# Performance work log

Hardware: AMD Instinct MI355X
Metric: run time of the kernel (lower is better)

The kernel has to match this reference:

```python
import jax, jax.numpy as jnp
import numpy as np

N_NODES = 100000
N_EDGES = 3200000
IN_FEATS = 512
HIDDEN = 16
NUM_CLASSES = 40


def setup_inputs() -> dict:
    key = jax.random.key(0)
    k1, k2, k3, k4, k5, k6 = jax.random.split(key, 6)
    x = jax.random.normal(k1, (N_NODES, IN_FEATS), dtype=jnp.float32)
    edge_index = jax.random.randint(k2, (2, N_EDGES), 0, N_NODES, dtype=jnp.int64)
    # Glorot-ish init for GCN weights
    W1 = jax.random.normal(k3, (IN_FEATS, HIDDEN), dtype=jnp.float32) / np.sqrt(IN_FEATS)
    b1 = jnp.zeros((HIDDEN,), dtype=jnp.float32)
    W2 = jax.random.normal(k4, (HIDDEN, NUM_CLASSES), dtype=jnp.float32) / np.sqrt(HIDDEN)
    b2 = jnp.zeros((NUM_CLASSES,), dtype=jnp.float32)
    return {"x": x, "edge_index": edge_index, "W1": W1, "b1": b1, "W2": W2, "b2": b2}


def _gcn_norm(edge_index, num_nodes):
    # Add self-loops (PyG GCNConv default), then symmetric normalization
    loops = jnp.arange(num_nodes, dtype=edge_index.dtype)
    src = jnp.concatenate([edge_index[0], loops])
    dst = jnp.concatenate([edge_index[1], loops])
    deg = jax.ops.segment_sum(jnp.ones_like(dst, dtype=jnp.float32), dst,
                              num_segments=num_nodes)
    dinv = jnp.where(deg > 0, jax.lax.rsqrt(deg), 0.0)
    norm = dinv[src] * dinv[dst]  # [E + N]
    return src, dst, norm


def _gcn_conv(x, W, b, src, dst, norm, num_nodes):
    h = x @ W                                   # transform first: [N, d_out]
    msg = h[src] * norm[:, None]                # gather + scale: [E+N, d_out]
    agg = jax.ops.segment_sum(msg, dst, num_segments=num_nodes)
    return agg + b


def reference(x, edge_index, W1, b1, W2, b2):
    num_nodes = x.shape[0]
    src, dst, norm = _gcn_norm(edge_index, num_nodes)
    h = _gcn_conv(x, W1, b1, src, dst, norm, num_nodes)
    h = jax.nn.relu(h)
    # F.dropout(training=self.training): eval mode -> identity (deterministic reference)
    h = _gcn_conv(h, W2, b2, src, dst, norm, num_nodes)
    return jax.nn.log_softmax(h, axis=1)
```

## Files before the change

### kernel.cpp

```cpp
#include <hip/hip_runtime.h>
#include <hip/hip_bf16.h>
#include <math.h>

#define N_NODES 100000
#define N_EDGES 3200000
#define IN_F    512
#define HID     16
#define NCLS    40
#define NB      2048
#define NPB     49
#define CAPW    2048
#define NBLK    256
#define EPB     12500

typedef unsigned short ushort_t;

__device__ __forceinline__ float bf16_to_f32(ushort_t u) {
    unsigned int b = ((unsigned int)u) << 16;
    return __uint_as_float(b);
}
__device__ __forceinline__ ushort_t f32_to_bf16(float f) {
    __hip_bfloat16 h = __float2bfloat16(f);
    return *(ushort_t*)&h;
}

__global__ __launch_bounds__(256) void k_detect(const int* __restrict__ ei,
                                                int* __restrict__ flag) {
    __shared__ int s_nz;
    if (threadIdx.x == 0) s_nz = 0;
    __syncthreads();
    int nz = 0;
    for (int i = threadIdx.x; i < 1024; i += 256)
        if (ei[2 * i + 1] != 0) nz = 1;
    if (nz) atomicOr(&s_nz, 1);
    __syncthreads();
    if (threadIdx.x == 0) flag[0] = s_nz ? 0 : 1;
}

__device__ __forceinline__ int load_edge(const void* ei, int is64, int idx) {
    if (is64) return (int)((const long long*)ei)[idx];
    return ((const int*)ei)[idx];
}

__global__ __launch_bounds__(256) void kInit(int* __restrict__ gcur) {
    int i = blockIdx.x * 256 + threadIdx.x;
    if (i < NB) gcur[i] = i * CAPW;
}

__global__ __launch_bounds__(256) void kB(const void* __restrict__ ei,
                                          const int* __restrict__ flag,
                                          int* __restrict__ gcur,
                                          int* __restrict__ binned) {
    __shared__ int hist[NB];
    __shared__ int base[NB];
    for (int i = threadIdx.x; i < NB; i += 256) hist[i] = 0;
    __syncthreads();
    int is64 = flag[0];
    int off0 = blockIdx.x * EPB;
    for (int i = threadIdx.x; i < EPB; i += 256) {
        int d = load_edge(ei, is64, N_EDGES + off0 + i);
        atomicAdd(&hist[d / NPB], 1);
    }
    __syncthreads();
    for (int i = threadIdx.x; i < NB; i += 256) {
        int c = hist[i];
        base[i] = c ? atomicAdd(&gcur[i], c) : 0;
        hist[i] = 0;
    }
    __syncthreads();
    for (int i = threadIdx.x; i < EPB; i += 256) {
        int s = load_edge(ei, is64, off0 + i);
        int d = load_edge(ei, is64, N_EDGES + off0 + i);
        int b = d / NPB;
        int o = atomicAdd(&hist[b], 1);
        binned[base[b] + o] = (s << 6) | (d - b * NPB);
    }
}

__global__ __launch_bounds__(256) void kSort(const int* __restrict__ gcur,
                                             int* __restrict__ binned,
                                             int* __restrict__ nstart,
                                             int* __restrict__ bend,
                                             float* __restrict__ dinv) {
    __shared__ int elist[CAPW];
    __shared__ int ih[NPB];
    __shared__ int lscan[NPB + 1];
    int b = blockIdx.x, tid = threadIdx.x;
    int beg = b * CAPW;
    int cnt = gcur[b] - beg;
    if (cnt > CAPW) cnt = CAPW;
    if (cnt < 0) cnt = 0;
    if (tid < NPB) ih[tid] = 0;
    __syncthreads();
    for (int k = tid; k < cnt; k += 256) {
        int p = binned[beg + k];
        elist[k] = p;
        atomicAdd(&ih[p & 63], 1);
    }
    __syncthreads();
    if (tid == 0) {
        int run = 0;
        for (int i = 0; i < NPB; ++i) { lscan[i] = run; run += ih[i]; }
        lscan[NPB] = run;
        bend[b] = beg + run;
    }
    __syncthreads();
    if (tid < NPB) {
        int n = b * NPB + tid;
        if (n < N_NODES) dinv[n] = rsqrtf((float)(ih[tid] + 1));
        nstart[n] = beg + lscan[tid];
        ih[tid] = lscan[tid];
    }
    __syncthreads();
    for (int k = tid; k < cnt; k += 256) {
        int p = elist[k];
        int pos = atomicAdd(&ih[p & 63], 1);
        binned[beg + pos] = p >> 6;
    }
}

__global__ __launch_bounds__(128) void k_gemm1(const float* __restrict__ x,
                                               const float* __restrict__ W1,
                                               const float* __restrict__ dinv,
                                               ushort_t* __restrict__ hsb) {
    __shared__ float Ws[IN_F * HID];
    for (int i = threadIdx.x; i < IN_F * HID; i += 128) Ws[i] = W1[i];
    __syncthreads();
    int n = blockIdx.x * 128 + threadIdx.x;
    if (n >= N_NODES) return;
    float acc[HID];
#pragma unroll
    for (int j = 0; j < HID; ++j) acc[j] = 0.0f;
    const float4* xr = (const float4*)(x + (size_t)n * IN_F);
    for (int k4 = 0; k4 < IN_F / 4; ++k4) {
        float4 xv = xr[k4];
        int kb = k4 * 4;
#pragma unroll
        for (int i = 0; i < 4; ++i) {
            float xs = (&xv.x)[i];
            const float4* wr = (const float4*)(Ws + (kb + i) * HID);
#pragma unroll
            for (int j4 = 0; j4 < 4; ++j4) {
                float4 w = wr[j4];
                acc[j4 * 4 + 0] += xs * w.x;
                acc[j4 * 4 + 1] += xs * w.y;
                acc[j4 * 4 + 2] += xs * w.z;
                acc[j4 * 4 + 3] += xs * w.w;
            }
        }
    }
    float di = dinv[n];
    ushort_t* hn = hsb + (size_t)n * HID;
#pragma unroll
    for (int j = 0; j < HID; ++j) hn[j] = f32_to_bf16(acc[j] * di);
}

__global__ __launch_bounds__(256) void kAgg1(const int* __restrict__ nstart,
                                             const int* __restrict__ bend,
                                             const int* __restrict__ sorted,
                                             const ushort_t* __restrict__ hsb,
                                             const float* __restrict__ dinv,
                                             const float* __restrict__ b1,
                                             ushort_t* __restrict__ h1sb) {
    int tid = threadIdx.x;
    int g = tid >> 4, lane = tid & 15;
    int n = blockIdx.x * 16 + g;
    int b = n / NPB, il = n - b * NPB;
    int beg = nstart[n];
    int end = (il == NPB - 1) ? bend[b] : nstart[n + 1];
    float acc = 0.0f;
    int k = beg;
    for (; k + 4 <= end; k += 4) {
        int s0 = sorted[k + 0], s1 = sorted[k + 1];
        int s2 = sorted[k + 2], s3 = sorted[k + 3];
        float v0 = bf16_to_f32(hsb[(size_t)s0 * HID + lane]);
        float v1 = bf16_to_f32(hsb[(size_t)s1 * HID + lane]);
        float v2 = bf16_to_f32(hsb[(size_t)s2 * HID + lane]);
        float v3 = bf16_to_f32(hsb[(size_t)s3 * HID + lane]);
        acc += (v0 + v1) + (v2 + v3);
    }
    for (; k < end; ++k)
        acc += bf16_to_f32(hsb[(size_t)sorted[k] * HID + lane]);
    float di = dinv[n];
    float self = bf16_to_f32(hsb[(size_t)n * HID + lane]);
    float v = di * (acc + self) + b1[lane];
    h1sb[(size_t)n * HID + lane] = f32_to_bf16(fmaxf(v, 0.0f) * di);
}

__global__ __launch_bounds__(256) void kAgg2(const int* __restrict__ nstart,
                                             const int* __restrict__ bend,
                                             const int* __restrict__ sorted,
                                             const ushort_t* __restrict__ h1sb,
                                             const float* __restrict__ dinv,
                                             float* __restrict__ agg2) {
    int tid = threadIdx.x;
    int g = tid >> 4, lane = tid & 15;
    int n = blockIdx.x * 16 + g;
    int b = n / NPB, il = n - b * NPB;
    int beg = nstart[n];
    int end = (il == NPB - 1) ? bend[b] : nstart[n + 1];
    float acc = 0.0f;
    int k = beg;
    for (; k + 4 <= end; k += 4) {
        int s0 = sorted[k + 0], s1 = sorted[k + 1];
        int s2 = sorted[k + 2], s3 = sorted[k + 3];
        float v0 = bf16_to_f32(h1sb[(size_t)s0 * HID + lane]);
        float v1 = bf16_to_f32(h1sb[(size_t)s1 * HID + lane]);
        float v2 = bf16_to_f32(h1sb[(size_t)s2 * HID + lane]);
        float v3 = bf16_to_f32(h1sb[(size_t)s3 * HID + lane]);
        acc += (v0 + v1) + (v2 + v3);
    }
    for (; k < end; ++k)
        acc += bf16_to_f32(h1sb[(size_t)sorted[k] * HID + lane]);
    float di = dinv[n];
    float self = bf16_to_f32(h1sb[(size_t)n * HID + lane]);
    agg2[(size_t)n * HID + lane] = di * (acc + self);
}

__global__ __launch_bounds__(128) void k_out(const float* __restrict__ agg2,
                                             const float* __restrict__ W2,
                                             const float* __restrict__ b2,
                                             float* __restrict__ out) {
    __shared__ float Ws[HID * NCLS];
    __shared__ float bs[NCLS];
    for (int i = threadIdx.x; i < HID * NCLS; i += 128) Ws[i] = W2[i];
    for (int i = threadIdx.x; i < NCLS; i += 128) bs[i] = b2[i];
    __syncthreads();
    int n = blockIdx.x * 128 + threadIdx.x;
    if (n >= N_NODES) return;
    float a[HID];
    const float4* ar = (const float4*)(agg2 + (size_t)n * HID);
#pragma unroll
    for (int q = 0; q < HID / 4; ++q) {
        float4 v = ar[q];
        a[q * 4 + 0] = v.x; a[q * 4 + 1] = v.y;
        a[q * 4 + 2] = v.z; a[q * 4 + 3] = v.w;
    }
    float logits[NCLS];
#pragma unroll
    for (int c = 0; c < NCLS; ++c) logits[c] = bs[c];
#pragma unroll
    for (int k = 0; k < HID; ++k) {
        float av = a[k];
        const float* wr = Ws + k * NCLS;
#pragma unroll
        for (int c = 0; c < NCLS; ++c) logits[c] += av * wr[c];
    }
    float m = logits[0];
#pragma unroll
    for (int c = 1; c < NCLS; ++c) m = fmaxf(m, logits[c]);
    float ssum = 0.0f;
#pragma unroll
    for (int c = 0; c < NCLS; ++c) ssum += expf(logits[c] - m);
    float lse = m + logf(ssum);
    float* on = out + (size_t)n * NCLS;
#pragma unroll
    for (int c = 0; c < NCLS; ++c) on[c] = logits[c] - lse;
}

extern "C" void kernel_launch(void* const* d_in, const int* in_sizes, int n_in,
                              void* d_out, int out_size, void* d_ws, size_t ws_size,
                              hipStream_t stream) {
    const float* x  = (const float*)d_in[0];
    const void*  ei = d_in[1];
    const float* W1 = (const float*)d_in[2];
    const float* b1 = (const float*)d_in[3];
    const float* W2 = (const float*)d_in[4];
    const float* b2 = (const float*)d_in[5];
    float* out = (float*)d_out;

    int*      iws    = (int*)d_ws;
    float*    fws    = (float*)d_ws;
    int*      gcur   = iws;
    int*      bend   = iws + 2048;
    int*      flag   = iws + 4096;
    float*    dinv   = fws + 8192;
    int*      nstart = iws + 108192;
    ushort_t* hsb    = (ushort_t*)(iws + 212992);
    ushort_t* h1sb   = (ushort_t*)(iws + 1012992);
    float*    agg2   = fws + 1812992;
    int*      binned = iws + 3412992;

    const int B = 256;

    k_detect<<<1, B, 0, stream>>>((const int*)ei, flag);
    kInit<<<(NB + B - 1) / B, B, 0, stream>>>(gcur);
    kB<<<NBLK, B, 0, stream>>>(ei, flag, gcur, binned);
    kSort<<<NB, B, 0, stream>>>(gcur, binned, nstart, bend, dinv);
    k_gemm1<<<(N_NODES + 127) / 128, 128, 0, stream>>>(x, W1, dinv, hsb);
    kAgg1<<<N_NODES / 16, B, 0, stream>>>(nstart, bend, binned, hsb, dinv, b1, h1sb);
    kAgg2<<<N_NODES / 16, B, 0, stream>>>(nstart, bend, binned, h1sb, dinv, agg2);
    k_out<<<(N_NODES + 127) / 128, 128, 0, stream>>>(agg2, W2, b2, out);
}
```

Baseline: 248.9 us.

## Fuse second aggregation with output projection and merge detect/init kernels

Merges the edge-format detection kernel into the cursor-init kernel, and fuses the second-layer aggregation with the W2 projection and log-softmax. Each 16-lane group keeps its node's aggregated features in shared memory, computes 40 logits spread across lanes, and reduces max and sum with shuffles. This removes the agg2 round trip through global memory and two kernel launches. The output stores are now split across lanes, and the extra shared-memory use and barrier may slightly reduce occupancy.

```diff
diff --git a/kernel.cpp b/kernel.cpp
--- a/kernel.cpp
+++ b/kernel.cpp
@@ -24,27 +24,27 @@
     return *(ushort_t*)&h;
 }
 
-__global__ __launch_bounds__(256) void k_detect(const int* __restrict__ ei,
-                                                int* __restrict__ flag) {
-    __shared__ int s_nz;
-    if (threadIdx.x == 0) s_nz = 0;
-    __syncthreads();
-    int nz = 0;
-    for (int i = threadIdx.x; i < 1024; i += 256)
-        if (ei[2 * i + 1] != 0) nz = 1;
-    if (nz) atomicOr(&s_nz, 1);
-    __syncthreads();
-    if (threadIdx.x == 0) flag[0] = s_nz ? 0 : 1;
-}
-
 __device__ __forceinline__ int load_edge(const void* ei, int is64, int idx) {
     if (is64) return (int)((const long long*)ei)[idx];
     return ((const int*)ei)[idx];
 }
 
-__global__ __launch_bounds__(256) void kInit(int* __restrict__ gcur) {
+__global__ __launch_bounds__(256) void kPre(const int* __restrict__ ei,
+                                            int* __restrict__ flag,
+                                            int* __restrict__ gcur) {
     int i = blockIdx.x * 256 + threadIdx.x;
     if (i < NB) gcur[i] = i * CAPW;
+    if (blockIdx.x == 0) {
+        __shared__ int s_nz;
+        if (threadIdx.x == 0) s_nz = 0;
+        __syncthreads();
+        int nz = 0;
+        for (int k = threadIdx.x; k < 1024; k += 256)
+            if (ei[2 * k + 1] != 0) nz = 1;
+        if (nz) atomicOr(&s_nz, 1);
+        __syncthreads();
+        if (threadIdx.x == 0) flag[0] = s_nz ? 0 : 1;
+    }
 }
 
 __global__ __launch_bounds__(256) void kB(const void* __restrict__ ei,
@@ -187,13 +187,21 @@
     h1sb[(size_t)n * HID + lane] = f32_to_bf16(fmaxf(v, 0.0f) * di);
 }
 
-__global__ __launch_bounds__(256) void kAgg2(const int* __restrict__ nstart,
-                                             const int* __restrict__ bend,
-                                             const int* __restrict__ sorted,
-                                             const ushort_t* __restrict__ h1sb,
-                                             const float* __restrict__ dinv,
-                                             float* __restrict__ agg2) {
+__global__ __launch_bounds__(256) void kAggOut(const int* __restrict__ nstart,
+                                               const int* __restrict__ bend,
+                                               const int* __restrict__ sorted,
+                                               const ushort_t* __restrict__ h1sb,
+                                               const float* __restrict__ dinv,
+                                               const float* __restrict__ W2,
+                                               const float* __restrict__ b2,
+                                               float* __restrict__ out) {
+    __shared__ float a2[16][HID + 1];
+    __shared__ float Ws[HID * NCLS];
+    __shared__ float bs[NCLS];
     int tid = threadIdx.x;
+    for (int i = tid; i < HID * NCLS; i += 256) Ws[i] = W2[i];
+    for (int i = tid; i < NCLS; i += 256) bs[i] = b2[i];
+
     int g = tid >> 4, lane = tid & 15;
     int n = blockIdx.x * 16 + g;
     int b = n / NPB, il = n - b * NPB;
@@ -214,48 +222,37 @@
         acc += bf16_to_f32(h1sb[(size_t)sorted[k] * HID + lane]);
     float di = dinv[n];
     float self = bf16_to_f32(h1sb[(size_t)n * HID + lane]);
-    agg2[(size_t)n * HID + lane] = di * (acc + self);
-}
-
-__global__ __launch_bounds__(128) void k_out(const float* __restrict__ agg2,
-                                             const float* __restrict__ W2,
-                                             const float* __restrict__ b2,
-                                             float* __restrict__ out) {
-    __shared__ float Ws[HID * NCLS];
-    __shared__ float bs[NCLS];
-    for (int i = threadIdx.x; i < HID * NCLS; i += 128) Ws[i] = W2[i];
-    for (int i = threadIdx.x; i < NCLS; i += 128) bs[i] = b2[i];
-    __syncthreads();
-    int n = blockIdx.x * 128 + threadIdx.x;
-    if (n >= N_NODES) return;
-    float a[HID];
-    const float4* ar = (const float4*)(agg2 + (size_t)n * HID);
-#pragma unroll
-    for (int q = 0; q < HID / 4; ++q) {
-        float4 v = ar[q];
-        a[q * 4 + 0] = v.x; a[q * 4 + 1] = v.y;
-        a[q * 4 + 2] = v.z; a[q * 4 + 3] = v.w;
-    }
-    float logits[NCLS];
-#pragma unroll
-    for (int c = 0; c < NCLS; ++c) logits[c] = bs[c];
-#pragma unroll
-    for (int k = 0; k < HID; ++k) {
-        float av = a[k];
-        const float* wr = Ws + k * NCLS;
-#pragma unroll
-        for (int c = 0; c < NCLS; ++c) logits[c] += av * wr[c];
-    }
-    float m = logits[0];
-#pragma unroll
-    for (int c = 1; c < NCLS; ++c) m = fmaxf(m, logits[c]);
-    float ssum = 0.0f;
-#pragma unroll
-    for (int c = 0; c < NCLS; ++c) ssum += expf(logits[c] - m);
-    float lse = m + logf(ssum);
-    float* on = out + (size_t)n * NCLS;
-#pragma unroll
-    for (int c = 0; c < NCLS; ++c) on[c] = logits[c] - lse;
+    a2[g][lane] = di * (acc + self);
+    __syncthreads();
+
+    int v = g;
+    int cidx = lane;
+    float av[HID];
+#pragma unroll
+    for (int j = 0; j < HID; ++j) av[j] = a2[v][j];
+    float l0 = bs[cidx], l1 = bs[cidx + 16];
+    float l2 = (cidx < 8) ? bs[cidx + 32] : -1e30f;
+#pragma unroll
+    for (int j = 0; j < HID; ++j) {
+        const float* wr = Ws + j * NCLS;
+        l0 += av[j] * wr[cidx];
+        l1 += av[j] * wr[cidx + 16];
+        if (cidx < 8) l2 += av[j] * wr[cidx + 32];
+    }
+    float m = fmaxf(l0, fmaxf(l1, l2));
+#pragma unroll
+    for (int off = 8; off >= 1; off >>= 1)
+        m = fmaxf(m, __shfl_xor(m, off, 16));
+    float e = expf(l0 - m) + expf(l1 - m) + ((cidx < 8) ? expf(l2 - m) : 0.0f);
+#pragma unroll
+    for (int off = 8; off >= 1; off >>= 1)
+        e += __shfl_xor(e, off, 16);
+    float lse = m + logf(e);
+    int nn = blockIdx.x * 16 + v;
+    float* on = out + (size_t)nn * NCLS;
+    on[cidx] = l0 - lse;
+    on[cidx + 16] = l1 - lse;
+    if (cidx < 8) on[cidx + 32] = l2 - lse;
 }
 
 extern "C" void kernel_launch(void* const* d_in, const int* in_sizes, int n_in,
@@ -278,17 +275,14 @@
     int*      nstart = iws + 108192;
     ushort_t* hsb    = (ushort_t*)(iws + 212992);
     ushort_t* h1sb   = (ushort_t*)(iws + 1012992);
-    float*    agg2   = fws + 1812992;
-    int*      binned = iws + 3412992;
+    int*      binned = iws + 1812992;
 
     const int B = 256;
 
-    k_detect<<<1, B, 0, stream>>>((const int*)ei, flag);
-    kInit<<<(NB + B - 1) / B, B, 0, stream>>>(gcur);
+    kPre<<<(NB + B - 1) / B, B, 0, stream>>>((const int*)ei, flag, gcur);
     kB<<<NBLK, B, 0, stream>>>(ei, flag, gcur, binned);
     kSort<<<NB, B, 0, stream>>>(gcur, binned, nstart, bend, dinv);
     k_gemm1<<<(N_NODES + 127) / 128, 128, 0, stream>>>(x, W1, dinv, hsb);
     kAgg1<<<N_NODES / 16, B, 0, stream>>>(nstart, bend, binned, hsb, dinv, b1, h1sb);
-    kAgg2<<<N_NODES / 16, B, 0, stream>>>(nstart, bend, binned, h1sb, dinv, agg2);
-    k_out<<<(N_NODES + 127) / 128, 128, 0, stream>>>(agg2, W2, b2, out);
-}
+    kAggOut<<<N_NODES / 16, B, 0, stream>>>(nstart, bend, binned, h1sb, dinv, W2, b2, out);
+}
```

Result: faster. 239.3 us (-3.9%).
